# Kernel optimization log

Measured on AMD Instinct MI355X. Metric: run time of the kernel, lower is better.

Reference implementation:

```python
import jax, jax.numpy as jnp
import numpy as np

NUM_GROUPS = 4
EPS = 1e-6


def group_norm(x, gamma, beta):
    # x: [b, c, h, w]; groups=4, eps=1e-6, affine
    b, c, h, w = x.shape
    g = NUM_GROUPS
    xg = x.reshape(b, g, c // g, h, w)
    mean = xg.mean(axis=(2, 3, 4), keepdims=True)
    var = xg.var(axis=(2, 3, 4), keepdims=True)
    xg = (xg - mean) / jnp.sqrt(var + EPS)
    xn = xg.reshape(b, c, h, w)
    return xn * gamma[None, :, None, None] + beta[None, :, None, None]


def conv1x1(x, w, bias):
    # 1x1 conv == per-pixel linear: w [out_c, in_c], bias [out_c]
    return jnp.einsum('bchw,oc->bohw', x, w) + bias[None, :, None, None]


def setup_inputs() -> dict:
    key = jax.random.key(0)
    ks = jax.random.split(key, 12)
    C = 256
    b, h, w = 8, 64, 64
    s = 1.0 / np.sqrt(C)
    inp = {
        'x': jax.random.normal(ks[0], (b, C, h, w), dtype=jnp.float32),
        'y': jax.random.normal(ks[1], (b, C, h, w), dtype=jnp.float32),
        'gn_gamma': jnp.ones((C,), dtype=jnp.float32),
        'gn_beta': jnp.zeros((C,), dtype=jnp.float32),
        'wq': jax.random.normal(ks[2], (C, C), dtype=jnp.float32) * s,
        'bq': jnp.zeros((C,), dtype=jnp.float32),
        'wk': jax.random.normal(ks[3], (C, C), dtype=jnp.float32) * s,
        'bk': jnp.zeros((C,), dtype=jnp.float32),
        'wv': jax.random.normal(ks[4], (C, C), dtype=jnp.float32) * s,
        'bv': jnp.zeros((C,), dtype=jnp.float32),
        'wp': jax.random.normal(ks[5], (C, C), dtype=jnp.float32) * s,
        'bp': jnp.zeros((C,), dtype=jnp.float32),
    }
    return inp


def reference(x, y, gn_gamma, gn_beta, wq, bq, wk, bk, wv, bv, wp, bp):
    # Shared norm applied to both x (query source) and y (key/value source)
    h_ = group_norm(x, gn_gamma, gn_beta)
    y_ = group_norm(y, gn_gamma, gn_beta)
    q = conv1x1(h_, wq, bq)  # [b, c, h, w]
    k = conv1x1(y_, wk, bk)  # [b, c, h1, w1]
    v = conv1x1(y_, wv, bv)
    b_, c, h, w = q.shape
    _, _, h1, w1 = k.shape
    qf = q.reshape(b_, c, h * w)      # [b, c, q]
    kf = k.reshape(b_, c, h1 * w1)    # [b, c, k]
    vf = v.reshape(b_, c, h1 * w1)    # [b, c, k]
    scale = jnp.asarray(int(c) ** (-0.5), dtype=qf.dtype)
    scores = jnp.einsum('bcq,bck->bqk', qf, kf) * scale  # [b, q, k]
    attn = jax.nn.softmax(scores, axis=2)
    out = jnp.einsum('bck,bqk->bcq', vf, attn)  # [b, c, q]
    out = out.reshape(b_, c, h, w)
    out = conv1x1(out, wp, bp)
    return x + out
```

## Files before the change

### kernel.cpp

```cpp
#include <hip/hip_runtime.h>
#include <math.h>


namespace {
constexpr int kB   = 8;
constexpr int kC   = 256;
constexpr int kCPG = 64;
constexpr int kHW  = 4096;
constexpr float kEps = 1e-6f;
}

typedef short bf16x8 __attribute__((ext_vector_type(8)));
typedef float f32x4  __attribute__((ext_vector_type(4)));

#define MFMA16(a, b, c) __builtin_amdgcn_mfma_f32_16x16x32_bf16((a), (b), (c), 0, 0, 0)

__device__ __forceinline__ unsigned short f2bf(float v) {
  unsigned u = __float_as_uint(v);
  u += 0x7FFFu + ((u >> 16) & 1u);
  return (unsigned short)(u >> 16);
}
__device__ __forceinline__ float bf2f(unsigned short h) {
  return __uint_as_float(((unsigned)h) << 16);
}

__global__ __launch_bounds__(256)
void wprep_kernel(const float* __restrict__ wq, const float* __restrict__ wk,
                  const float* __restrict__ wv, const float* __restrict__ wp,
                  unsigned short* __restrict__ Wqb, unsigned short* __restrict__ Wkb,
                  unsigned short* __restrict__ Wvb, unsigned short* __restrict__ Wpb) {
  int i = (blockIdx.x * 256 + threadIdx.x) * 4;
  {
    float4 a = *(const float4*)(wq + i);
    ushort4 h = {f2bf(a.x), f2bf(a.y), f2bf(a.z), f2bf(a.w)};
    *(ushort4*)(Wqb + i) = h;
  }
  {
    float4 a = *(const float4*)(wk + i);
    ushort4 h = {f2bf(a.x), f2bf(a.y), f2bf(a.z), f2bf(a.w)};
    *(ushort4*)(Wkb + i) = h;
  }
  {
    float4 a = *(const float4*)(wv + i);
    ushort4 h = {f2bf(a.x), f2bf(a.y), f2bf(a.z), f2bf(a.w)};
    *(ushort4*)(Wvb + i) = h;
  }
  {
    float4 a = *(const float4*)(wp + i);
    ushort4 h = {f2bf(a.x), f2bf(a.y), f2bf(a.z), f2bf(a.w)};
    *(ushort4*)(Wpb + i) = h;
  }
}

__global__ __launch_bounds__(256)
void gn_part_kernel(const float* __restrict__ x, const float* __restrict__ y,
                    float* __restrict__ part) {
  int blk   = blockIdx.x;
  int grp   = blk >> 3;
  int chunk = blk & 7;
  int g = grp & 3;
  int b = (grp >> 2) & 7;
  int t = grp >> 5;
  const float* src = (t == 0 ? x : y) + ((size_t)b * kC + (size_t)g * kCPG) * kHW
                     + (size_t)chunk * 32768;
  float sum = 0.f, ssq = 0.f;
  for (int i = threadIdx.x * 4; i < 32768; i += 1024) {
    float4 v = *(const float4*)(src + i);
    sum += v.x + v.y + v.z + v.w;
    ssq += v.x * v.x + v.y * v.y + v.z * v.z + v.w * v.w;
  }
  #pragma unroll
  for (int off = 32; off > 0; off >>= 1) {
    sum += __shfl_down(sum, off);
    ssq += __shfl_down(ssq, off);
  }
  __shared__ float rs[4], rq[4];
  int lane = threadIdx.x & 63, w = threadIdx.x >> 6;
  if (lane == 0) { rs[w] = sum; rq[w] = ssq; }
  __syncthreads();
  if (threadIdx.x == 0) {
    part[blk * 2]     = rs[0] + rs[1] + rs[2] + rs[3];
    part[blk * 2 + 1] = rq[0] + rq[1] + rq[2] + rq[3];
  }
}

__global__ __launch_bounds__(64)
void gn_fin_kernel(const float* __restrict__ part,
                   const float* __restrict__ gamma, const float* __restrict__ beta,
                   float* __restrict__ scaleX, float* __restrict__ shiftX,
                   float* __restrict__ scaleY, float* __restrict__ shiftY) {
  int grp = blockIdx.x;
  int g = grp & 3;
  int b = (grp >> 2) & 7;
  int t = grp >> 5;
  float s = 0.f, q = 0.f;
  #pragma unroll
  for (int j = 0; j < 8; ++j) {
    s += part[(grp * 8 + j) * 2];
    q += part[(grp * 8 + j) * 2 + 1];
  }
  const float N = (float)(kCPG * kHW);
  float mean = s / N;
  float var  = q / N - mean * mean;
  float rstd = rsqrtf(var + kEps);
  int c = g * kCPG + threadIdx.x;
  float sc = gamma[c] * rstd;
  float sh = beta[c] - mean * sc;
  if (t == 0) { scaleX[b * kC + c] = sc; shiftX[b * kC + c] = sh; }
  else        { scaleY[b * kC + c] = sc; shiftY[b * kC + c] = sh; }
}

__global__ __launch_bounds__(256, 2)
void qkv_mfma_kernel(const float* __restrict__ x, const float* __restrict__ y,
                     const unsigned short* __restrict__ Wqb,
                     const unsigned short* __restrict__ Wkb,
                     const unsigned short* __restrict__ Wvb,
                     const float* __restrict__ bq, const float* __restrict__ bk,
                     const float* __restrict__ bv,
                     const float* __restrict__ scaleX, const float* __restrict__ shiftX,
                     const float* __restrict__ scaleY, const float* __restrict__ shiftY,
                     unsigned short* __restrict__ Qo, unsigned short* __restrict__ Ko,
                     unsigned short* __restrict__ Vo) {
  int z  = blockIdx.y;
  int bi = blockIdx.x;
  int pt = bi & 63;
  int b  = bi >> 6;
  int pbase = pt * 64;
  const float* X = (z == 0 ? x : y) + (size_t)b * kC * kHW;
  const unsigned short* Wb = (z == 0 ? Wqb : (z == 1 ? Wkb : Wvb));
  const float* bias = (z == 0 ? bq : (z == 1 ? bk : bv));
  const float* SC   = (z == 0 ? scaleX : scaleY) + b * kC;
  const float* SH   = (z == 0 ? shiftX : shiftY) + b * kC;

  __shared__ short Ws[256][40];
  __shared__ short Xs[64][40];
  __shared__ float Xt[32][68];

  int tid  = threadIdx.x;
  int lane = tid & 63;
  int w    = tid >> 6;
  int lrow = lane & 15;
  int lgrp = lane >> 4;

  f32x4 acc[4][4];
  #pragma unroll
  for (int i = 0; i < 4; ++i)
    #pragma unroll
    for (int j = 0; j < 4; ++j) acc[i][j] = (f32x4){0.f, 0.f, 0.f, 0.f};

  for (int c0 = 0; c0 < kC; c0 += 32) {
    __syncthreads();
    {
      const int4* s4 = (const int4*)(Wb + (size_t)tid * kC + c0);
      *(int4*)&Ws[tid][0]  = s4[0];
      *(int4*)&Ws[tid][8]  = s4[1];
      *(int4*)&Ws[tid][16] = s4[2];
      *(int4*)&Ws[tid][24] = s4[3];
    }
    {
      int c  = tid >> 3;
      int p8 = (tid & 7) * 8;
      const float* s = X + (size_t)(c0 + c) * kHW + pbase + p8;
      float sc = SC[c0 + c], sh = SH[c0 + c];
      float4 a0 = *(const float4*)(s);
      float4 a1 = *(const float4*)(s + 4);
      float4 r0 = make_float4(fmaf(a0.x, sc, sh), fmaf(a0.y, sc, sh), fmaf(a0.z, sc, sh), fmaf(a0.w, sc, sh));
      float4 r1 = make_float4(fmaf(a1.x, sc, sh), fmaf(a1.y, sc, sh), fmaf(a1.z, sc, sh), fmaf(a1.w, sc, sh));
      *(float4*)&Xt[c][p8]     = r0;
      *(float4*)&Xt[c][p8 + 4] = r1;
    }
    __syncthreads();
    {
      int p  = tid & 63;
      int cs = (tid >> 6) * 8;
      short hh[8];
      #pragma unroll
      for (int i = 0; i < 8; ++i) hh[i] = (short)f2bf(Xt[cs + i][p]);
      *(bf16x8*)&Xs[p][cs] = *(bf16x8*)hh;
    }
    __syncthreads();

    if (z < 2) {
      bf16x8 am[4], bn[4];
      #pragma unroll
      for (int mt = 0; mt < 4; ++mt)
        am[mt] = *(const bf16x8*)&Ws[w * 64 + mt * 16 + lrow][lgrp * 8];
      #pragma unroll
      for (int nt = 0; nt < 4; ++nt)
        bn[nt] = *(const bf16x8*)&Xs[nt * 16 + lrow][lgrp * 8];
      #pragma unroll
      for (int mt = 0; mt < 4; ++mt)
        #pragma unroll
        for (int nt = 0; nt < 4; ++nt)
          acc[mt][nt] = MFMA16(am[mt], bn[nt], acc[mt][nt]);
    } else {
      bf16x8 am[4], bn[4];
      #pragma unroll
      for (int mt = 0; mt < 4; ++mt)
        am[mt] = *(const bf16x8*)&Xs[mt * 16 + lrow][lgrp * 8];
      #pragma unroll
      for (int nt = 0; nt < 4; ++nt)
        bn[nt] = *(const bf16x8*)&Ws[w * 64 + nt * 16 + lrow][lgrp * 8];
      #pragma unroll
      for (int mt = 0; mt < 4; ++mt)
        #pragma unroll
        for (int nt = 0; nt < 4; ++nt)
          acc[mt][nt] = MFMA16(am[mt], bn[nt], acc[mt][nt]);
    }
  }

  if (z < 2) {
    float osc = (z == 0) ? 0.0625f : 1.0f;
    unsigned short* T = ((z == 0) ? Qo : Ko) + (size_t)b * kHW * kC;
    #pragma unroll
    for (int mt = 0; mt < 4; ++mt) {
      int o0 = w * 64 + mt * 16 + lgrp * 4;
      float4 b4 = *(const float4*)&bias[o0];
      #pragma unroll
      for (int nt = 0; nt < 4; ++nt) {
        int p = pbase + nt * 16 + lrow;
        ushort4 hh;
        hh.x = f2bf((acc[mt][nt][0] + b4.x) * osc);
        hh.y = f2bf((acc[mt][nt][1] + b4.y) * osc);
        hh.z = f2bf((acc[mt][nt][2] + b4.z) * osc);
        hh.w = f2bf((acc[mt][nt][3] + b4.w) * osc);
        *(ushort4*)&T[(size_t)p * kC + o0] = hh;
      }
    }
  } else {
    unsigned short* Vb = Vo + (size_t)b * kHW * kC;
    #pragma unroll
    for (int nt = 0; nt < 4; ++nt) {
      int o = w * 64 + nt * 16 + lrow;
      float bo = bias[o];
      #pragma unroll
      for (int mt = 0; mt < 4; ++mt) {
        int p0 = pbase + mt * 16 + lgrp * 4;
        ushort4 hh;
        hh.x = f2bf(acc[mt][nt][0] + bo);
        hh.y = f2bf(acc[mt][nt][1] + bo);
        hh.z = f2bf(acc[mt][nt][2] + bo);
        hh.w = f2bf(acc[mt][nt][3] + bo);
        *(ushort4*)&Vb[(size_t)o * kHW + p0] = hh;
      }
    }
  }
}

__global__ __launch_bounds__(256, 2)
void flash_mfma_kernel(const unsigned short* __restrict__ Q,
                       const unsigned short* __restrict__ K,
                       const unsigned short* __restrict__ V,
                       float* __restrict__ Ot) {
  int bid = blockIdx.x;
  int b  = bid & 7;
  int qt = bid >> 3;
  const size_t toff = (size_t)b * kHW * kC;
  const unsigned short* Qb = Q + toff;
  const unsigned short* Kb = K + toff;
  const unsigned short* Vb = V + toff;
  float* O = Ot + toff;

  __shared__ short K_s[64][264];
  __shared__ short V_s[256][72];
  __shared__ short P_s[64][72];

  int tid  = threadIdx.x;
  int lane = tid & 63;
  int w    = tid >> 6;
  int lrow = lane & 15;
  int lgrp = lane >> 4;

  bf16x8 qf[8];
  {
    int qrow = qt * 64 + w * 16 + lrow;
    const unsigned short* qb = Qb + (size_t)qrow * kC + lgrp * 8;
    #pragma unroll
    for (int cc = 0; cc < 8; ++cc) qf[cc] = *(const bf16x8*)(qb + cc * 32);
  }

  int krow0 = tid >> 5;
  int kcol  = (tid & 31) * 8;
  int vc0   = tid >> 3;
  int vpart = (tid & 7) * 8;

  f32x4 accO[16];
  #pragma unroll
  for (int nt = 0; nt < 16; ++nt) accO[nt] = (f32x4){0.f, 0.f, 0.f, 0.f};
  float m_[4], l_[4];
  #pragma unroll
  for (int r = 0; r < 4; ++r) { m_[r] = -1e30f; l_[r] = 0.f; }

  for (int kt = 0; kt < 64; ++kt) {
    int kbase = kt * 64;
    __syncthreads();
    #pragma unroll
    for (int rep = 0; rep < 8; ++rep) {
      *(int4*)&K_s[krow0 + rep * 8][kcol] =
          *(const int4*)(Kb + (size_t)(kbase + krow0 + rep * 8) * kC + kcol);
      *(int4*)&V_s[vc0 + rep * 32][vpart] =
          *(const int4*)(Vb + (size_t)(vc0 + rep * 32) * kHW + kbase + vpart);
    }
    __syncthreads();

    f32x4 s0 = (f32x4){0.f, 0.f, 0.f, 0.f};
    f32x4 s1 = (f32x4){0.f, 0.f, 0.f, 0.f};
    f32x4 s2 = (f32x4){0.f, 0.f, 0.f, 0.f};
    f32x4 s3 = (f32x4){0.f, 0.f, 0.f, 0.f};
    #pragma unroll
    for (int cc = 0; cc < 8; ++cc) {
      int coff = cc * 32 + lgrp * 8;
      bf16x8 k0 = *(const bf16x8*)&K_s[lrow][coff];
      bf16x8 k1 = *(const bf16x8*)&K_s[16 + lrow][coff];
      bf16x8 k2 = *(const bf16x8*)&K_s[32 + lrow][coff];
      bf16x8 k3 = *(const bf16x8*)&K_s[48 + lrow][coff];
      s0 = MFMA16(qf[cc], k0, s0);
      s1 = MFMA16(qf[cc], k1, s1);
      s2 = MFMA16(qf[cc], k2, s2);
      s3 = MFMA16(qf[cc], k3, s3);
    }

    int prow = w * 16 + lgrp * 4;
    #pragma unroll
    for (int r = 0; r < 4; ++r) {
      float mx = fmaxf(fmaxf(s0[r], s1[r]), fmaxf(s2[r], s3[r]));
      mx = fmaxf(mx, __shfl_xor(mx, 1));
      mx = fmaxf(mx, __shfl_xor(mx, 2));
      mx = fmaxf(mx, __shfl_xor(mx, 4));
      mx = fmaxf(mx, __shfl_xor(mx, 8));
      float mn = fmaxf(m_[r], mx);
      float f  = __expf(m_[r] - mn);
      unsigned short u0 = f2bf(__expf(s0[r] - mn));
      unsigned short u1 = f2bf(__expf(s1[r] - mn));
      unsigned short u2 = f2bf(__expf(s2[r] - mn));
      unsigned short u3 = f2bf(__expf(s3[r] - mn));
      float sum = (bf2f(u0) + bf2f(u1)) + (bf2f(u2) + bf2f(u3));
      sum += __shfl_xor(sum, 1);
      sum += __shfl_xor(sum, 2);
      sum += __shfl_xor(sum, 4);
      sum += __shfl_xor(sum, 8);
      l_[r] = l_[r] * f + sum;
      m_[r] = mn;
      P_s[prow + r][lrow]      = (short)u0;
      P_s[prow + r][16 + lrow] = (short)u1;
      P_s[prow + r][32 + lrow] = (short)u2;
      P_s[prow + r][48 + lrow] = (short)u3;
      #pragma unroll
      for (int nt = 0; nt < 16; ++nt) accO[nt][r] *= f;
    }

    bf16x8 pa0 = *(const bf16x8*)&P_s[w * 16 + lrow][lgrp * 8];
    bf16x8 pa1 = *(const bf16x8*)&P_s[w * 16 + lrow][32 + lgrp * 8];
    #pragma unroll
    for (int nt = 0; nt < 16; ++nt) {
      bf16x8 vb0 = *(const bf16x8*)&V_s[nt * 16 + lrow][lgrp * 8];
      bf16x8 vb1 = *(const bf16x8*)&V_s[nt * 16 + lrow][32 + lgrp * 8];
      accO[nt] = MFMA16(pa0, vb0, accO[nt]);
      accO[nt] = MFMA16(pa1, vb1, accO[nt]);
    }
  }

  float inv[4];
  #pragma unroll
  for (int r = 0; r < 4; ++r) inv[r] = 1.0f / l_[r];
  int qbase = qt * 64 + w * 16 + lgrp * 4;
  #pragma unroll
  for (int nt = 0; nt < 16; ++nt) {
    #pragma unroll
    for (int r = 0; r < 4; ++r) {
      O[(size_t)(qbase + r) * kC + nt * 16 + lrow] = accO[nt][r] * inv[r];
    }
  }
}

__global__ __launch_bounds__(256, 2)
void proj_mfma_kernel(const float* __restrict__ Ot,
                      const unsigned short* __restrict__ Wpb,
                      const float* __restrict__ bp, const float* __restrict__ x,
                      float* __restrict__ out) {
  int bi = blockIdx.x;
  int pt = bi & 63;
  int b  = bi >> 6;
  int pbase = pt * 64;
  const float* Ob = Ot + (size_t)b * kHW * kC;

  __shared__ short Ws[256][40];
  __shared__ short Os[64][40];

  int tid  = threadIdx.x;
  int lane = tid & 63;
  int w    = tid >> 6;
  int lrow = lane & 15;
  int lgrp = lane >> 4;

  f32x4 acc[4][4];
  #pragma unroll
  for (int i = 0; i < 4; ++i)
    #pragma unroll
    for (int j = 0; j < 4; ++j) acc[i][j] = (f32x4){0.f, 0.f, 0.f, 0.f};

  for (int c0 = 0; c0 < kC; c0 += 32) {
    __syncthreads();
    {
      const int4* s4 = (const int4*)(Wpb + (size_t)tid * kC + c0);
      *(int4*)&Ws[tid][0]  = s4[0];
      *(int4*)&Ws[tid][8]  = s4[1];
      *(int4*)&Ws[tid][16] = s4[2];
      *(int4*)&Ws[tid][24] = s4[3];
    }
    {
      int p  = tid >> 2;
      int c8 = (tid & 3) * 8;
      const float* s = Ob + (size_t)(pbase + p) * kC + c0 + c8;
      float4 a0 = *(const float4*)(s);
      float4 a1 = *(const float4*)(s + 4);
      short hh[8] = {(short)f2bf(a0.x), (short)f2bf(a0.y), (short)f2bf(a0.z), (short)f2bf(a0.w),
                     (short)f2bf(a1.x), (short)f2bf(a1.y), (short)f2bf(a1.z), (short)f2bf(a1.w)};
      *(bf16x8*)&Os[p][c8] = *(bf16x8*)hh;
    }
    __syncthreads();

    bf16x8 am[4], bn[4];
    #pragma unroll
    for (int mt = 0; mt < 4; ++mt)
      am[mt] = *(const bf16x8*)&Os[mt * 16 + lrow][lgrp * 8];
    #pragma unroll
    for (int nt = 0; nt < 4; ++nt)
      bn[nt] = *(const bf16x8*)&Ws[w * 64 + nt * 16 + lrow][lgrp * 8];
    #pragma unroll
    for (int mt = 0; mt < 4; ++mt)
      #pragma unroll
      for (int nt = 0; nt < 4; ++nt)
        acc[mt][nt] = MFMA16(am[mt], bn[nt], acc[mt][nt]);
  }

  #pragma unroll
  for (int nt = 0; nt < 4; ++nt) {
    int o = w * 64 + nt * 16 + lrow;
    float bo = bp[o];
    #pragma unroll
    for (int mt = 0; mt < 4; ++mt) {
      int p0 = pbase + mt * 16 + lgrp * 4;
      const float* xr   = x   + ((size_t)b * kC + o) * kHW + p0;
      float*       orow = out + ((size_t)b * kC + o) * kHW + p0;
      float4 xv = *(const float4*)xr;
      float4 v = make_float4(acc[mt][nt][0] + bo + xv.x, acc[mt][nt][1] + bo + xv.y,
                             acc[mt][nt][2] + bo + xv.z, acc[mt][nt][3] + bo + xv.w);
      *(float4*)orow = v;
    }
  }
}

extern "C" void kernel_launch(void* const* d_in, const int* in_sizes, int n_in,
                              void* d_out, int out_size, void* d_ws, size_t ws_size,
                              hipStream_t stream) {
  (void)in_sizes; (void)n_in; (void)out_size;
  const float* x     = (const float*)d_in[0];
  const float* y     = (const float*)d_in[1];
  const float* gamma = (const float*)d_in[2];
  const float* beta  = (const float*)d_in[3];
  const float* wq    = (const float*)d_in[4];
  const float* bq    = (const float*)d_in[5];
  const float* wk    = (const float*)d_in[6];
  const float* bk    = (const float*)d_in[7];
  const float* wv    = (const float*)d_in[8];
  const float* bv    = (const float*)d_in[9];
  const float* wp    = (const float*)d_in[10];
  const float* bp    = (const float*)d_in[11];
  float* out = (float*)d_out;

  char* ws = (char*)d_ws;
  size_t bsz = (size_t)kB * kHW * kC * sizeof(unsigned short);
  size_t fsz = (size_t)kB * kHW * kC * sizeof(float);
  size_t wsz = (size_t)kC * kC * sizeof(unsigned short);
  size_t need = 3 * bsz + fsz + 4 * wsz
              + 4 * (size_t)kB * kC * sizeof(float) + 1024 * sizeof(float);
  if (ws_size < need) return;

  unsigned short* Qb  = (unsigned short*)(ws);
  unsigned short* Kb  = (unsigned short*)(ws + 1 * bsz);
  unsigned short* Vb  = (unsigned short*)(ws + 2 * bsz);
  float*          Ot  = (float*)(ws + 3 * bsz);
  unsigned short* Wqb = (unsigned short*)(ws + 3 * bsz + fsz);
  unsigned short* Wkb = (unsigned short*)(ws + 3 * bsz + fsz + 1 * wsz);
  unsigned short* Wvb = (unsigned short*)(ws + 3 * bsz + fsz + 2 * wsz);
  unsigned short* Wpb = (unsigned short*)(ws + 3 * bsz + fsz + 3 * wsz);
  float* scaleX = (float*)(ws + 3 * bsz + fsz + 4 * wsz);
  float* shiftX = scaleX + kB * kC;
  float* scaleY = shiftX + kB * kC;
  float* shiftY = scaleY + kB * kC;
  float* part   = shiftY + kB * kC;

  wprep_kernel<<<dim3(64), dim3(256), 0, stream>>>(
      wq, wk, wv, wp, Wqb, Wkb, Wvb, Wpb);
  gn_part_kernel<<<dim3(512), dim3(256), 0, stream>>>(x, y, part);
  gn_fin_kernel<<<dim3(64), dim3(64), 0, stream>>>(
      part, gamma, beta, scaleX, shiftX, scaleY, shiftY);
  qkv_mfma_kernel<<<dim3(kB * 64, 3), dim3(256), 0, stream>>>(
      x, y, Wqb, Wkb, Wvb, bq, bk, bv, scaleX, shiftX, scaleY, shiftY,
      Qb, Kb, Vb);
  flash_mfma_kernel<<<dim3(kB * 64), dim3(256), 0, stream>>>(Qb, Kb, Vb, Ot);
  proj_mfma_kernel<<<dim3(kB * 64), dim3(256), 0, stream>>>(Ot, Wpb, bp, x, out);
}
```

Before: 466.2 us.

## Switch flash attention to 32x32 MFMA tiles with split-KV and merged partials

The flash kernel now uses 32x32x16 bf16 MFMA, so each wave owns 32 query rows instead of 16. Each block now covers 128 queries and half of the key range, with 32-key tiles. Per-half unnormalized outputs and (max, sum) statistics go to workspace, and the projection kernel merges the two halves with log-sum-exp weights before converting to bf16. This aims to raise MFMA efficiency and cut K/V reloads per query. In exchange it doubles the fp32 intermediate written and read, and the projection kernel reads twice as much data.

```diff
diff --git a/kernel.cpp b/kernel.cpp
--- a/kernel.cpp
+++ b/kernel.cpp
@@ -12,8 +12,10 @@
 
 typedef short bf16x8 __attribute__((ext_vector_type(8)));
 typedef float f32x4  __attribute__((ext_vector_type(4)));
+typedef float f32x16 __attribute__((ext_vector_type(16)));
 
 #define MFMA16(a, b, c) __builtin_amdgcn_mfma_f32_16x16x32_bf16((a), (b), (c), 0, 0, 0)
+#define MFMA32(a, b, c) __builtin_amdgcn_mfma_f32_32x32x16_bf16((a), (b), (c), 0, 0, 0)
 
 __device__ __forceinline__ unsigned short f2bf(float v) {
   unsigned u = __float_as_uint(v);
@@ -251,130 +253,127 @@
 void flash_mfma_kernel(const unsigned short* __restrict__ Q,
                        const unsigned short* __restrict__ K,
                        const unsigned short* __restrict__ V,
-                       float* __restrict__ Ot) {
-  int bid = blockIdx.x;
-  int b  = bid & 7;
-  int qt = bid >> 3;
+                       float* __restrict__ Opart, float2* __restrict__ ML) {
+  int bid  = blockIdx.x;
+  int b    = bid & 7;
+  int qt   = (bid >> 3) & 31;
+  int half = bid >> 8;
   const size_t toff = (size_t)b * kHW * kC;
   const unsigned short* Qb = Q + toff;
   const unsigned short* Kb = K + toff;
   const unsigned short* Vb = V + toff;
-  float* O = Ot + toff;
-
-  __shared__ short K_s[64][264];
-  __shared__ short V_s[256][72];
-  __shared__ short P_s[64][72];
+  float*  Op  = Opart + ((size_t)half * kB + b) * kHW * kC;
+  float2* MLp = ML + ((size_t)half * kB + b) * kHW;
+  int kstart = half * 2048;
+
+  __shared__ short K_s[32][264];
+  __shared__ short V_s[256][40];
+  __shared__ short P_s[4][32][40];
 
   int tid  = threadIdx.x;
   int lane = tid & 63;
   int w    = tid >> 6;
-  int lrow = lane & 15;
-  int lgrp = lane >> 4;
-
-  bf16x8 qf[8];
+  int l31  = lane & 31;
+  int hi   = lane >> 5;
+
+  bf16x8 qf[16];
   {
-    int qrow = qt * 64 + w * 16 + lrow;
-    const unsigned short* qb = Qb + (size_t)qrow * kC + lgrp * 8;
-    #pragma unroll
-    for (int cc = 0; cc < 8; ++cc) qf[cc] = *(const bf16x8*)(qb + cc * 32);
+    int qrow = qt * 128 + w * 32 + l31;
+    const unsigned short* qp = Qb + (size_t)qrow * kC + hi * 8;
+    #pragma unroll
+    for (int cc = 0; cc < 16; ++cc) qf[cc] = *(const bf16x8*)(qp + cc * 16);
   }
 
   int krow0 = tid >> 5;
   int kcol  = (tid & 31) * 8;
-  int vc0   = tid >> 3;
-  int vpart = (tid & 7) * 8;
-
-  f32x4 accO[16];
-  #pragma unroll
-  for (int nt = 0; nt < 16; ++nt) accO[nt] = (f32x4){0.f, 0.f, 0.f, 0.f};
-  float m_[4], l_[4];
-  #pragma unroll
-  for (int r = 0; r < 4; ++r) { m_[r] = -1e30f; l_[r] = 0.f; }
+  int vc0   = tid >> 2;
+  int vpart = (tid & 3) * 8;
+
+  f32x16 accO[8];
+  #pragma unroll
+  for (int ct = 0; ct < 8; ++ct)
+    #pragma unroll
+    for (int r = 0; r < 16; ++r) accO[ct][r] = 0.f;
+  float m_[16], l_[16];
+  #pragma unroll
+  for (int r = 0; r < 16; ++r) { m_[r] = -1e30f; l_[r] = 0.f; }
 
   for (int kt = 0; kt < 64; ++kt) {
-    int kbase = kt * 64;
-    __syncthreads();
-    #pragma unroll
-    for (int rep = 0; rep < 8; ++rep) {
+    int kbase = kstart + kt * 32;
+    __syncthreads();
+    #pragma unroll
+    for (int rep = 0; rep < 4; ++rep) {
       *(int4*)&K_s[krow0 + rep * 8][kcol] =
           *(const int4*)(Kb + (size_t)(kbase + krow0 + rep * 8) * kC + kcol);
-      *(int4*)&V_s[vc0 + rep * 32][vpart] =
-          *(const int4*)(Vb + (size_t)(vc0 + rep * 32) * kHW + kbase + vpart);
-    }
-    __syncthreads();
-
-    f32x4 s0 = (f32x4){0.f, 0.f, 0.f, 0.f};
-    f32x4 s1 = (f32x4){0.f, 0.f, 0.f, 0.f};
-    f32x4 s2 = (f32x4){0.f, 0.f, 0.f, 0.f};
-    f32x4 s3 = (f32x4){0.f, 0.f, 0.f, 0.f};
-    #pragma unroll
-    for (int cc = 0; cc < 8; ++cc) {
-      int coff = cc * 32 + lgrp * 8;
-      bf16x8 k0 = *(const bf16x8*)&K_s[lrow][coff];
-      bf16x8 k1 = *(const bf16x8*)&K_s[16 + lrow][coff];
-      bf16x8 k2 = *(const bf16x8*)&K_s[32 + lrow][coff];
-      bf16x8 k3 = *(const bf16x8*)&K_s[48 + lrow][coff];
-      s0 = MFMA16(qf[cc], k0, s0);
-      s1 = MFMA16(qf[cc], k1, s1);
-      s2 = MFMA16(qf[cc], k2, s2);
-      s3 = MFMA16(qf[cc], k3, s3);
-    }
-
-    int prow = w * 16 + lgrp * 4;
-    #pragma unroll
-    for (int r = 0; r < 4; ++r) {
-      float mx = fmaxf(fmaxf(s0[r], s1[r]), fmaxf(s2[r], s3[r]));
+      *(int4*)&V_s[vc0 + rep * 64][vpart] =
+          *(const int4*)(Vb + (size_t)(vc0 + rep * 64) * kHW + kbase + vpart);
+    }
+    __syncthreads();
+
+    f32x16 S;
+    #pragma unroll
+    for (int r = 0; r < 16; ++r) S[r] = 0.f;
+    #pragma unroll
+    for (int cc = 0; cc < 16; ++cc) {
+      bf16x8 kf = *(const bf16x8*)&K_s[l31][cc * 16 + hi * 8];
+      S = MFMA32(qf[cc], kf, S);
+    }
+
+    #pragma unroll
+    for (int r = 0; r < 16; ++r) {
+      float mx = S[r];
       mx = fmaxf(mx, __shfl_xor(mx, 1));
       mx = fmaxf(mx, __shfl_xor(mx, 2));
       mx = fmaxf(mx, __shfl_xor(mx, 4));
       mx = fmaxf(mx, __shfl_xor(mx, 8));
+      mx = fmaxf(mx, __shfl_xor(mx, 16));
       float mn = fmaxf(m_[r], mx);
-      float f  = __expf(m_[r] - mn);
-      unsigned short u0 = f2bf(__expf(s0[r] - mn));
-      unsigned short u1 = f2bf(__expf(s1[r] - mn));
-      unsigned short u2 = f2bf(__expf(s2[r] - mn));
-      unsigned short u3 = f2bf(__expf(s3[r] - mn));
-      float sum = (bf2f(u0) + bf2f(u1)) + (bf2f(u2) + bf2f(u3));
+      float fr = __expf(m_[r] - mn);
+      unsigned short u = f2bf(__expf(S[r] - mn));
+      float sum = bf2f(u);
       sum += __shfl_xor(sum, 1);
       sum += __shfl_xor(sum, 2);
       sum += __shfl_xor(sum, 4);
       sum += __shfl_xor(sum, 8);
-      l_[r] = l_[r] * f + sum;
+      sum += __shfl_xor(sum, 16);
+      l_[r] = l_[r] * fr + sum;
       m_[r] = mn;
-      P_s[prow + r][lrow]      = (short)u0;
-      P_s[prow + r][16 + lrow] = (short)u1;
-      P_s[prow + r][32 + lrow] = (short)u2;
-      P_s[prow + r][48 + lrow] = (short)u3;
-      #pragma unroll
-      for (int nt = 0; nt < 16; ++nt) accO[nt][r] *= f;
-    }
-
-    bf16x8 pa0 = *(const bf16x8*)&P_s[w * 16 + lrow][lgrp * 8];
-    bf16x8 pa1 = *(const bf16x8*)&P_s[w * 16 + lrow][32 + lgrp * 8];
-    #pragma unroll
-    for (int nt = 0; nt < 16; ++nt) {
-      bf16x8 vb0 = *(const bf16x8*)&V_s[nt * 16 + lrow][lgrp * 8];
-      bf16x8 vb1 = *(const bf16x8*)&V_s[nt * 16 + lrow][32 + lgrp * 8];
-      accO[nt] = MFMA16(pa0, vb0, accO[nt]);
-      accO[nt] = MFMA16(pa1, vb1, accO[nt]);
-    }
-  }
-
-  float inv[4];
-  #pragma unroll
-  for (int r = 0; r < 4; ++r) inv[r] = 1.0f / l_[r];
-  int qbase = qt * 64 + w * 16 + lgrp * 4;
-  #pragma unroll
-  for (int nt = 0; nt < 16; ++nt) {
-    #pragma unroll
-    for (int r = 0; r < 4; ++r) {
-      O[(size_t)(qbase + r) * kC + nt * 16 + lrow] = accO[nt][r] * inv[r];
+      int crow = (r & 3) + 8 * (r >> 2) + 4 * hi;
+      P_s[w][crow][l31] = (short)u;
+      #pragma unroll
+      for (int ct = 0; ct < 8; ++ct) accO[ct][r] *= fr;
+    }
+
+    bf16x8 pa0 = *(const bf16x8*)&P_s[w][l31][hi * 8];
+    bf16x8 pa1 = *(const bf16x8*)&P_s[w][l31][16 + hi * 8];
+    #pragma unroll
+    for (int ct = 0; ct < 8; ++ct) {
+      bf16x8 v0 = *(const bf16x8*)&V_s[ct * 32 + l31][hi * 8];
+      bf16x8 v1 = *(const bf16x8*)&V_s[ct * 32 + l31][16 + hi * 8];
+      accO[ct] = MFMA32(pa0, v0, accO[ct]);
+      accO[ct] = MFMA32(pa1, v1, accO[ct]);
+    }
+  }
+
+  int q0 = qt * 128 + w * 32;
+  #pragma unroll
+  for (int r = 0; r < 16; ++r) {
+    int q = q0 + (r & 3) + 8 * (r >> 2) + 4 * hi;
+    float* orow = Op + (size_t)q * kC + l31;
+    #pragma unroll
+    for (int ct = 0; ct < 8; ++ct) orow[ct * 32] = accO[ct][r];
+  }
+  if (l31 == 0) {
+    #pragma unroll
+    for (int r = 0; r < 16; ++r) {
+      int q = q0 + (r & 3) + 8 * (r >> 2) + 4 * hi;
+      MLp[q] = make_float2(m_[r], l_[r]);
     }
   }
 }
 
 __global__ __launch_bounds__(256, 2)
-void proj_mfma_kernel(const float* __restrict__ Ot,
+void proj_mfma_kernel(const float* __restrict__ Opart, const float2* __restrict__ ML,
                       const unsigned short* __restrict__ Wpb,
                       const float* __restrict__ bp, const float* __restrict__ x,
                       float* __restrict__ out) {
@@ -382,7 +381,10 @@
   int pt = bi & 63;
   int b  = bi >> 6;
   int pbase = pt * 64;
-  const float* Ob = Ot + (size_t)b * kHW * kC;
+  const float* Oa = Opart + (size_t)b * kHW * kC;
+  const float* Obf = Opart + ((size_t)kB + b) * kHW * kC;
+  const float2* MLa = ML + (size_t)b * kHW;
+  const float2* MLb = ML + ((size_t)kB + b) * kHW;
 
   __shared__ short Ws[256][40];
   __shared__ short Os[64][40];
@@ -392,6 +394,17 @@
   int w    = tid >> 6;
   int lrow = lane & 15;
   int lgrp = lane >> 4;
+
+  int prow = tid >> 2;
+  int qrow = pbase + prow;
+  float2 mla = MLa[qrow];
+  float2 mlb = MLb[qrow];
+  float mm = fmaxf(mla.x, mlb.x);
+  float wa = __expf(mla.x - mm);
+  float wb = __expf(mlb.x - mm);
+  float inv = 1.0f / (mla.y * wa + mlb.y * wb);
+  wa *= inv;
+  wb *= inv;
 
   f32x4 acc[4][4];
   #pragma unroll
@@ -409,14 +422,19 @@
       *(int4*)&Ws[tid][24] = s4[3];
     }
     {
-      int p  = tid >> 2;
       int c8 = (tid & 3) * 8;
-      const float* s = Ob + (size_t)(pbase + p) * kC + c0 + c8;
-      float4 a0 = *(const float4*)(s);
-      float4 a1 = *(const float4*)(s + 4);
-      short hh[8] = {(short)f2bf(a0.x), (short)f2bf(a0.y), (short)f2bf(a0.z), (short)f2bf(a0.w),
-                     (short)f2bf(a1.x), (short)f2bf(a1.y), (short)f2bf(a1.z), (short)f2bf(a1.w)};
-      *(bf16x8*)&Os[p][c8] = *(bf16x8*)hh;
+      const float* sa = Oa  + (size_t)qrow * kC + c0 + c8;
+      const float* sb = Obf + (size_t)qrow * kC + c0 + c8;
+      float4 a0 = *(const float4*)(sa);
+      float4 a1 = *(const float4*)(sa + 4);
+      float4 b0 = *(const float4*)(sb);
+      float4 b1 = *(const float4*)(sb + 4);
+      short hh[8] = {
+        (short)f2bf(a0.x * wa + b0.x * wb), (short)f2bf(a0.y * wa + b0.y * wb),
+        (short)f2bf(a0.z * wa + b0.z * wb), (short)f2bf(a0.w * wa + b0.w * wb),
+        (short)f2bf(a1.x * wa + b1.x * wb), (short)f2bf(a1.y * wa + b1.y * wb),
+        (short)f2bf(a1.z * wa + b1.z * wb), (short)f2bf(a1.w * wa + b1.w * wb)};
+      *(bf16x8*)&Os[prow][c8] = *(bf16x8*)hh;
     }
     __syncthreads();
 
@@ -473,19 +491,21 @@
   size_t bsz = (size_t)kB * kHW * kC * sizeof(unsigned short);
   size_t fsz = (size_t)kB * kHW * kC * sizeof(float);
   size_t wsz = (size_t)kC * kC * sizeof(unsigned short);
-  size_t need = 3 * bsz + fsz + 4 * wsz
+  size_t mlsz = (size_t)2 * kB * kHW * sizeof(float2);
+  size_t need = 3 * bsz + 2 * fsz + 4 * wsz + mlsz
               + 4 * (size_t)kB * kC * sizeof(float) + 1024 * sizeof(float);
   if (ws_size < need) return;
 
   unsigned short* Qb  = (unsigned short*)(ws);
   unsigned short* Kb  = (unsigned short*)(ws + 1 * bsz);
   unsigned short* Vb  = (unsigned short*)(ws + 2 * bsz);
-  float*          Ot  = (float*)(ws + 3 * bsz);
-  unsigned short* Wqb = (unsigned short*)(ws + 3 * bsz + fsz);
-  unsigned short* Wkb = (unsigned short*)(ws + 3 * bsz + fsz + 1 * wsz);
-  unsigned short* Wvb = (unsigned short*)(ws + 3 * bsz + fsz + 2 * wsz);
-  unsigned short* Wpb = (unsigned short*)(ws + 3 * bsz + fsz + 3 * wsz);
-  float* scaleX = (float*)(ws + 3 * bsz + fsz + 4 * wsz);
+  float*          Opart = (float*)(ws + 3 * bsz);
+  unsigned short* Wqb = (unsigned short*)(ws + 3 * bsz + 2 * fsz);
+  unsigned short* Wkb = (unsigned short*)(ws + 3 * bsz + 2 * fsz + 1 * wsz);
+  unsigned short* Wvb = (unsigned short*)(ws + 3 * bsz + 2 * fsz + 2 * wsz);
+  unsigned short* Wpb = (unsigned short*)(ws + 3 * bsz + 2 * fsz + 3 * wsz);
+  float2* ML    = (float2*)(ws + 3 * bsz + 2 * fsz + 4 * wsz);
+  float* scaleX = (float*)(ws + 3 * bsz + 2 * fsz + 4 * wsz + mlsz);
   float* shiftX = scaleX + kB * kC;
   float* scaleY = shiftX + kB * kC;
   float* shiftY = scaleY + kB * kC;
@@ -499,6 +519,7 @@
   qkv_mfma_kernel<<<dim3(kB * 64, 3), dim3(256), 0, stream>>>(
       x, y, Wqb, Wkb, Wvb, bq, bk, bv, scaleX, shiftX, scaleY, shiftY,
       Qb, Kb, Vb);
-  flash_mfma_kernel<<<dim3(kB * 64), dim3(256), 0, stream>>>(Qb, Kb, Vb, Ot);
-  proj_mfma_kernel<<<dim3(kB * 64), dim3(256), 0, stream>>>(Ot, Wpb, bp, x, out);
-}
+  flash_mfma_kernel<<<dim3(512), dim3(256), 0, stream>>>(Qb, Kb, Vb, Opart, ML);
+  proj_mfma_kernel<<<dim3(kB * 64), dim3(256), 0, stream>>>(
+      Opart, ML, Wpb, bp, x, out);
+}
```

Result: slower. 667.0 us (+43.1%).
